# Kernel optimization log

Hardware: AMD Instinct MI355X
Metric: run time of the kernel (lower is better)

Reference implementation:

```python
import jax, jax.numpy as jnp
import numpy as np

B, L, C = 512, 2048, 32  # batch, seq_len, num_labels


def setup_inputs() -> dict:
    key = jax.random.key(0)
    k1, k2, k3 = jax.random.split(key, 3)
    emissions = jax.random.normal(k1, (B, L, C), dtype=jnp.float32)
    tags = jax.random.randint(k2, (B, L), 0, C, dtype=jnp.int32)
    mask = jnp.ones((B, L), dtype=jnp.int32)
    # learned parameter: transitions (num_labels, num_labels)
    transitions = jax.random.normal(k3, (C, C), dtype=jnp.float32)
    return {"emissions": emissions, "transitions": transitions, "tags": tags, "mask": mask}


def _crf_nll(emissions, transitions, tags, mask):
    Bn, Ln, Cn = emissions.shape
    maskf = mask.astype(emissions.dtype)

    # ---- gold-path score (vectorized over the t loop) ----
    # emit[b,t] = emissions[b,t,tags[b,t]] for t in [0, L-2]
    emit = jnp.take_along_axis(emissions[:, : Ln - 1], tags[:, : Ln - 1, None], axis=2)[..., 0]
    # trans[b,t] = transitions[tags[b,t], tags[b,t+1]]
    trans = transitions[tags[:, : Ln - 1], tags[:, 1:]]
    score = jnp.sum(emit * maskf[:, : Ln - 1] + trans * maskf[:, 1:], axis=1)

    msum = jnp.sum(mask, axis=1)
    last_idx = jnp.clip(msum - 1, 0)  # index of last valid tag
    last_tag = jnp.take_along_axis(tags, last_idx[:, None], axis=1)[:, 0]
    le_t = jnp.clip(msum, 1) - 1
    last_emission = emissions[jnp.arange(Bn), le_t, last_tag]
    score = score + last_emission

    # ---- log-partition via forward algorithm (lax.scan over time) ----
    # Faithful to source: alpha_t[b,n,p] = alpha[b,p] + transitions[n,p] + emit[b,n],
    # reduced over p; the source's mask line is an algebraic no-op (a*m + a*(1-m) = a).
    def step(alpha, emit_t):
        # alpha: (B, C) over prev label p; emit_t: (B, C) over next label n
        alpha_new = jax.nn.logsumexp(alpha[:, None, :] + transitions[None, :, :], axis=2) + emit_t
        return alpha_new, None

    alpha0 = emissions[:, 0]                      # (B, C)
    em_rest = jnp.swapaxes(emissions[:, 1:], 0, 1)  # (L-1, B, C)
    alpha, _ = jax.lax.scan(step, alpha0, em_rest)
    log_Z = jax.nn.logsumexp(alpha, axis=1)       # (B,)

    return jnp.mean(log_Z - score)


def reference(emissions, transitions, tags, mask):
    return _crf_nll(emissions, transitions, tags, mask)
```

## Files before the change

kernel.cpp:

```cpp
#include <hip/hip_runtime.h>
#include <stdint.h>

typedef short bf16x8 __attribute__((ext_vector_type(8)));
typedef float f32x16 __attribute__((ext_vector_type(16)));

#define LOG2E 1.44269504088896340736f
#define LN2f  0.69314718055994530942f

constexpr int Bn = 512;
constexpr int Ln = 2048;
constexpr int Cn = 32;
constexpr int NSEG = 64;
constexpr int SEGLEN = 32;
constexpr int WARM = 16;
constexpr int NGRP = 16;
constexpr int WPB  = 4;

__device__ __forceinline__ uint32_t pack2_bf16(float lo, float hi) {
    uint32_t a = __float_as_uint(lo) + 0x8000u;
    uint32_t b = __float_as_uint(hi) + 0x8000u;
    return __builtin_amdgcn_perm(b, a, 0x07060302u);
}

__global__ __launch_bounds__(256, 1) void crf_scan(
    const float* __restrict__ emis, const float* __restrict__ trans,
    const int* __restrict__ tags, const int* __restrict__ mask,
    float* __restrict__ dDelta, float* __restrict__ dScore, int* __restrict__ dMsum)
{
    __shared__ float Tlds[Cn * Cn];
    const int lane = threadIdx.x & 63;
    const int wid  = threadIdx.x >> 6;
    const int h    = lane >> 5;
    const int bl   = lane & 31;
    const int unit = blockIdx.x * WPB + wid;
    const int g    = unit & (NGRP - 1);
    const int s    = unit >> 4;
    const int b    = g * 32 + bl;
    const size_t eb = (size_t)b * Ln * Cn;
    const size_t tB = (size_t)b * Ln;

    for (int i = threadIdx.x; i < Cn * Cn; i += 256) Tlds[i] = trans[i];
    __syncthreads();

    bf16x8 A1, A2;
    {
        float e1[8], e2[8];
        #pragma unroll
        for (int j = 0; j < 8; ++j) {
            int c1 = 4 * h + (j & 3) + 8 * (j >> 2);
            e1[j] = __expf(trans[bl * Cn + c1]);
            e2[j] = __expf(trans[bl * Cn + c1 + 16]);
        }
        union { uint32_t u[4]; bf16x8 v; } ua, ub;
        #pragma unroll
        for (int q = 0; q < 4; ++q) {
            ua.u[q] = pack2_bf16(e1[2*q], e1[2*q+1]);
            ub.u[q] = pack2_bf16(e2[2*q], e2[2*q+1]);
        }
        A1 = ua.v; A2 = ub.v;
    }

    const f32x16 zeroC = {0.f,0.f,0.f,0.f,0.f,0.f,0.f,0.f,0.f,0.f,0.f,0.f,0.f,0.f,0.f,0.f};

    f32x16 Dv;
    bf16x8 B1, B2;
    float offF = 0.f;
    float adj  = 0.f;
    float score = 0.f;
    int   msum = 0;
    int   prevTag = 0;
    float4 buf[8][4];
    int tcur[8], mcur[8];

    const int t0 = (s == 0) ? 0 : s * SEGLEN - WARM;

    auto loadEm = [&](int t, float4 (&dst)[4]) {
        const float4* p = (const float4*)(emis + eb + (size_t)t * Cn + 4 * h);
        dst[0] = p[0]; dst[1] = p[2]; dst[2] = p[4]; dst[3] = p[6];
    };

    auto packB = [&]() {
        union { uint32_t u[4]; bf16x8 v; } p1, p2;
        #pragma unroll
        for (int q = 0; q < 4; ++q) {
            p1.u[q] = pack2_bf16(Dv[2*q],     Dv[2*q + 1]);
            p2.u[q] = pack2_bf16(Dv[8 + 2*q], Dv[8 + 2*q + 1]);
        }
        B1 = p1.v; B2 = p2.v;
    };

    auto initStep = [&](const float4 (&bu)[4]) {
        #pragma unroll
        for (int q = 0; q < 4; ++q) {
            Dv[4*q+0] = __expf(bu[q].x);
            Dv[4*q+1] = __expf(bu[q].y);
            Dv[4*q+2] = __expf(bu[q].z);
            Dv[4*q+3] = __expf(bu[q].w);
        }
        packB();
    };

    auto stepMfma = [&](const float4 (&bu)[4], float a) {
        f32x16 acc = __builtin_amdgcn_mfma_f32_32x32x16_bf16(A1, B1, zeroC, 0, 0, 0);
        acc = __builtin_amdgcn_mfma_f32_32x32x16_bf16(A2, B2, acc, 0, 0, 0);
        #pragma unroll
        for (int q = 0; q < 4; ++q) {
            float x0 = exp2f(fmaf(bu[q].x, LOG2E, a));
            float x1 = exp2f(fmaf(bu[q].y, LOG2E, a));
            float x2 = exp2f(fmaf(bu[q].z, LOG2E, a));
            float x3 = exp2f(fmaf(bu[q].w, LOG2E, a));
            Dv[4*q+0] = acc[4*q+0] * x0;
            Dv[4*q+1] = acc[4*q+1] * x1;
            Dv[4*q+2] = acc[4*q+2] * x2;
            Dv[4*q+3] = acc[4*q+3] * x3;
        }
        packB();
    };

    auto renorm = [&]() {
        float m0 = fmaxf(fmaxf(Dv[0], Dv[1]),  fmaxf(Dv[2],  Dv[3]));
        float m1 = fmaxf(fmaxf(Dv[4], Dv[5]),  fmaxf(Dv[6],  Dv[7]));
        float m2 = fmaxf(fmaxf(Dv[8], Dv[9]),  fmaxf(Dv[10], Dv[11]));
        float m3 = fmaxf(fmaxf(Dv[12],Dv[13]), fmaxf(Dv[14], Dv[15]));
        float m  = fmaxf(fmaxf(m0, m1), fmaxf(m2, m3));
        m = fmaxf(m, __shfl_xor(m, 32, 64));
        int k = (int)((__float_as_uint(m) >> 23) & 0xffu) - 126;
        offF += (float)k * LN2f;
        adj = -(float)k;
    };

    auto sumD = [&]() {
        float t = 0.f;
        #pragma unroll
        for (int r = 0; r < 16; ++r) t += Dv[r];
        t += __shfl_xor(t, 32, 64);
        return t;
    };

    auto loadTagsMask = [&](int t) {
        int4 a0 = *(const int4*)(tags + tB + t);
        int4 a1 = *(const int4*)(tags + tB + t + 4);
        int4 c0 = *(const int4*)(mask + tB + t);
        int4 c1 = *(const int4*)(mask + tB + t + 4);
        tcur[0]=a0.x; tcur[1]=a0.y; tcur[2]=a0.z; tcur[3]=a0.w;
        tcur[4]=a1.x; tcur[5]=a1.y; tcur[6]=a1.z; tcur[7]=a1.w;
        mcur[0]=c0.x; mcur[1]=c0.y; mcur[2]=c0.z; mcur[3]=c0.w;
        mcur[4]=c1.x; mcur[5]=c1.y; mcur[6]=c1.z; mcur[7]=c1.w;
    };

    auto realBlock = [&](int tb) {
        int tn = min(tb + 8, Ln - 8);
        int4 a0 = *(const int4*)(tags + tB + tn);
        int4 a1 = *(const int4*)(tags + tB + tn + 4);
        int4 c0 = *(const int4*)(mask + tB + tn);
        int4 c1 = *(const int4*)(mask + tB + tn + 4);
        float gv[8];
        #pragma unroll
        for (int u = 0; u < 8; ++u)
            gv[u] = emis[eb + (size_t)(tb + u) * Cn + tcur[u]];
        #pragma unroll
        for (int u = 0; u < 8; ++u) {
            stepMfma(buf[u], (u == 0) ? adj : 0.f);
            loadEm(min(tb + u + 8, Ln - 1), buf[u]);
            float fm = (float)mcur[u];
            msum += mcur[u];
            score += fm * Tlds[(prevTag << 5) + tcur[u]];
            if (tb + u < Ln - 1) score += fm * gv[u];
            prevTag = tcur[u];
        }
        adj = 0.f;
        tcur[0]=a0.x; tcur[1]=a0.y; tcur[2]=a0.z; tcur[3]=a0.w;
        tcur[4]=a1.x; tcur[5]=a1.y; tcur[6]=a1.z; tcur[7]=a1.w;
        mcur[0]=c0.x; mcur[1]=c0.y; mcur[2]=c0.z; mcur[3]=c0.w;
        mcur[4]=c1.x; mcur[5]=c1.y; mcur[6]=c1.z; mcur[7]=c1.w;
    };

    #pragma unroll
    for (int u = 0; u < 8; ++u) loadEm(t0 + u, buf[u]);

    if (s == 0) {
        loadTagsMask(0);
        initStep(buf[0]);
        loadEm(8, buf[0]);
        float g0 = emis[eb + tcur[0]];
        score += (float)mcur[0] * g0;
        msum += mcur[0];
        prevTag = tcur[0];
        float gv[8];
        #pragma unroll
        for (int u = 1; u < 8; ++u) gv[u] = emis[eb + (size_t)u * Cn + tcur[u]];
        #pragma unroll
        for (int u = 1; u < 8; ++u) {
            stepMfma(buf[u], 0.f);
            loadEm(u + 8, buf[u]);
            float fm = (float)mcur[u];
            msum += mcur[u];
            score += fm * Tlds[(prevTag << 5) + tcur[u]];
            score += fm * gv[u];
            prevTag = tcur[u];
        }
        loadTagsMask(8);
        renorm();
        constexpr int NB0 = (SEGLEN - 8) / 8;
        #pragma unroll 1
        for (int blk = 0; blk < NB0; ++blk) {
            realBlock(8 + 8 * blk);
            if (blk < NB0 - 1) renorm();
        }
    } else {
        initStep(buf[0]);
        loadEm(t0 + 8, buf[0]);
        #pragma unroll
        for (int u = 1; u < 8; ++u) {
            stepMfma(buf[u], 0.f);
            loadEm(t0 + 8 + u, buf[u]);
        }
        renorm();
        prevTag = tags[tB + s * SEGLEN - 1];
        loadTagsMask(s * SEGLEN);
        #pragma unroll
        for (int u = 0; u < 8; ++u) {
            stepMfma(buf[u], (u == 0) ? adj : 0.f);
            loadEm(min(t0 + u + 16, Ln - 1), buf[u]);
        }
        adj = 0.f;
        float S = sumD();
        adj = -__log2f(S);
        offF = 0.f;
        constexpr int NB = SEGLEN / 8;
        #pragma unroll 1
        for (int blk = 0; blk < NB; ++blk) {
            realBlock(s * SEGLEN + 8 * blk);
            if (blk < NB - 1) renorm();
        }
    }

    float Sf = sumD();
    float delta = offF + __logf(Sf);
    if (lane < 32) {
        dDelta[s * Bn + b] = delta;
        dScore[s * Bn + b] = score;
        dMsum [s * Bn + b] = msum;
    }
}

__global__ void crf_final(const float* __restrict__ dDelta, const float* __restrict__ dScore,
                          const int* __restrict__ dMsum, const int* __restrict__ tags,
                          const float* __restrict__ emis, float* __restrict__ out)
{
    __shared__ float red[8];
    int b = threadIdx.x;
    float lz = 0.f, sc = 0.f; int ms = 0;
    #pragma unroll 8
    for (int s2 = 0; s2 < NSEG; ++s2) {
        lz += dDelta[s2 * Bn + b];
        sc += dScore[s2 * Bn + b];
        ms += dMsum [s2 * Bn + b];
    }
    int last_idx = max(ms - 1, 0);
    int le_t     = max(ms, 1) - 1;
    int lt = tags[(size_t)b * Ln + last_idx];
    float le = emis[((size_t)b * Ln + le_t) * Cn + lt];
    float val = lz - (sc + le);
    #pragma unroll
    for (int o = 32; o > 0; o >>= 1) val += __shfl_down(val, o, 64);
    if ((b & 63) == 0) red[b >> 6] = val;
    __syncthreads();
    if (b == 0) {
        float t = 0.f;
        #pragma unroll
        for (int w = 0; w < 8; ++w) t += red[w];
        out[0] = t * (1.0f / (float)Bn);
    }
}

extern "C" void kernel_launch(void* const* d_in, const int* in_sizes, int n_in,
                              void* d_out, int out_size, void* d_ws, size_t ws_size,
                              hipStream_t stream)
{
    const float* emis  = (const float*)d_in[0];
    const float* trans = (const float*)d_in[1];
    const int*   tags  = (const int*)d_in[2];
    const int*   mask  = (const int*)d_in[3];
    float* wsf = (float*)d_ws;
    float* dDelta = wsf;
    float* dScore = wsf + NSEG * Bn;
    int*   dMsum  = (int*)(wsf + 2 * NSEG * Bn);
    crf_scan<<<(NGRP * NSEG) / WPB, 64 * WPB, 0, stream>>>(emis, trans, tags, mask, dDelta, dScore, dMsum);
    crf_final<<<1, Bn, 0, stream>>>(dDelta, dScore, dMsum, tags, emis, (float*)d_out);
}
```

Baseline: 240.5 us.

## Stream emissions via async global-to-LDS loads and split gold-score into separate kernel

The scan kernel now prefetches each timestep's emission tile into a swizzled per-wave LDS ring of depth 8 using global_load_lds, with a manual vmcnt wait, instead of holding register buffers. Gold-path score and mask-sum work moves out of the serial scan into a new per-batch parallel kernel that also reduces the segment deltas. The aim is to cut register pressure and per-step latency in the recurrence and to give the score computation full parallelism. The cost is an extra kernel launch, a second pass over tags and emissions, and reliance on a hand-tuned vmcnt count being correct.

```diff
diff --git a/kernel.cpp b/kernel.cpp
--- a/kernel.cpp
+++ b/kernel.cpp
@@ -15,6 +15,7 @@
 constexpr int WARM = 16;
 constexpr int NGRP = 16;
 constexpr int WPB  = 4;
+constexpr int DEPTH = 8;
 
 __device__ __forceinline__ uint32_t pack2_bf16(float lo, float hi) {
     uint32_t a = __float_as_uint(lo) + 0x8000u;
@@ -22,25 +23,39 @@
     return __builtin_amdgcn_perm(b, a, 0x07060302u);
 }
 
+__device__ __forceinline__ void gload16(const float* g, float* l) {
+    __builtin_amdgcn_global_load_lds(
+        (__attribute__((address_space(1))) void*)g,
+        (__attribute__((address_space(3))) void*)l,
+        16, 0, 0);
+}
+
 __global__ __launch_bounds__(256, 1) void crf_scan(
     const float* __restrict__ emis, const float* __restrict__ trans,
-    const int* __restrict__ tags, const int* __restrict__ mask,
-    float* __restrict__ dDelta, float* __restrict__ dScore, int* __restrict__ dMsum)
+    float* __restrict__ dDelta)
 {
-    __shared__ float Tlds[Cn * Cn];
+    __shared__ float ELDS[WPB][DEPTH][1024];
     const int lane = threadIdx.x & 63;
     const int wid  = threadIdx.x >> 6;
     const int h    = lane >> 5;
     const int bl   = lane & 31;
+    const int bl7  = bl & 7;
     const int unit = blockIdx.x * WPB + wid;
     const int g    = unit & (NGRP - 1);
     const int s    = unit >> 4;
     const int b    = g * 32 + bl;
-    const size_t eb = (size_t)b * Ln * Cn;
-    const size_t tB = (size_t)b * Ln;
-
-    for (int i = threadIdx.x; i < Cn * Cn; i += 256) Tlds[i] = trans[i];
-    __syncthreads();
+
+    size_t gqb[4];
+    {
+        const int lr = lane >> 3;
+        const int lc = lane & 7;
+        #pragma unroll
+        for (int q = 0; q < 4; ++q) {
+            int br = 8 * q + lr;
+            int sg = lc ^ lr;
+            gqb[q] = (size_t)(g * 32 + br) * Ln * Cn + (size_t)(sg * 4);
+        }
+    }
 
     bf16x8 A1, A2;
     {
@@ -66,17 +81,24 @@
     bf16x8 B1, B2;
     float offF = 0.f;
     float adj  = 0.f;
-    float score = 0.f;
-    int   msum = 0;
-    int   prevTag = 0;
-    float4 buf[8][4];
-    int tcur[8], mcur[8];
 
     const int t0 = (s == 0) ? 0 : s * SEGLEN - WARM;
-
-    auto loadEm = [&](int t, float4 (&dst)[4]) {
-        const float4* p = (const float4*)(emis + eb + (size_t)t * Cn + 4 * h);
-        dst[0] = p[0]; dst[1] = p[2]; dst[2] = p[4]; dst[3] = p[6];
+    const int nsteps = (s == 0) ? SEGLEN : (SEGLEN + WARM);
+
+    auto issueTile = [&](int t, int slot) {
+        #pragma unroll
+        for (int q = 0; q < 4; ++q) {
+            const float* gp = emis + gqb[q] + (size_t)t * Cn;
+            gload16(gp, &ELDS[wid][slot][q * 256]);
+        }
+    };
+
+    auto readFrag = [&](int slot, float4 (&bu)[4]) {
+        #pragma unroll
+        for (int q = 0; q < 4; ++q) {
+            int c16 = (h + 2 * q) ^ bl7;
+            bu[q] = *(const float4*)&ELDS[wid][slot][bl * 32 + c16 * 4];
+        }
     };
 
     auto packB = [&]() {
@@ -89,18 +111,12 @@
         B1 = p1.v; B2 = p2.v;
     };
 
-    auto initStep = [&](const float4 (&bu)[4]) {
-        #pragma unroll
-        for (int q = 0; q < 4; ++q) {
-            Dv[4*q+0] = __expf(bu[q].x);
-            Dv[4*q+1] = __expf(bu[q].y);
-            Dv[4*q+2] = __expf(bu[q].z);
-            Dv[4*q+3] = __expf(bu[q].w);
-        }
-        packB();
-    };
-
-    auto stepMfma = [&](const float4 (&bu)[4], float a) {
+    auto pclamp = [&](int t) { return (t > Ln - 1) ? (Ln - 1) : t; };
+
+    auto stepConsume = [&](int idx, float a) {
+        asm volatile("s_waitcnt vmcnt(28)" ::: "memory");
+        float4 bu[4];
+        readFrag(idx & (DEPTH - 1), bu);
         f32x16 acc = __builtin_amdgcn_mfma_f32_32x32x16_bf16(A1, B1, zeroC, 0, 0, 0);
         acc = __builtin_amdgcn_mfma_f32_32x32x16_bf16(A2, B2, acc, 0, 0, 0);
         #pragma unroll
@@ -115,6 +131,24 @@
             Dv[4*q+3] = acc[4*q+3] * x3;
         }
         packB();
+        asm volatile("" ::: "memory");
+        issueTile(pclamp(t0 + idx + DEPTH), idx & (DEPTH - 1));
+    };
+
+    auto initConsume = [&](int idx) {
+        asm volatile("s_waitcnt vmcnt(28)" ::: "memory");
+        float4 bu[4];
+        readFrag(idx & (DEPTH - 1), bu);
+        #pragma unroll
+        for (int q = 0; q < 4; ++q) {
+            Dv[4*q+0] = __expf(bu[q].x);
+            Dv[4*q+1] = __expf(bu[q].y);
+            Dv[4*q+2] = __expf(bu[q].z);
+            Dv[4*q+3] = __expf(bu[q].w);
+        }
+        packB();
+        asm volatile("" ::: "memory");
+        issueTile(pclamp(t0 + idx + DEPTH), idx & (DEPTH - 1));
     };
 
     auto renorm = [&]() {
@@ -137,101 +171,40 @@
         return t;
     };
 
-    auto loadTagsMask = [&](int t) {
-        int4 a0 = *(const int4*)(tags + tB + t);
-        int4 a1 = *(const int4*)(tags + tB + t + 4);
-        int4 c0 = *(const int4*)(mask + tB + t);
-        int4 c1 = *(const int4*)(mask + tB + t + 4);
-        tcur[0]=a0.x; tcur[1]=a0.y; tcur[2]=a0.z; tcur[3]=a0.w;
-        tcur[4]=a1.x; tcur[5]=a1.y; tcur[6]=a1.z; tcur[7]=a1.w;
-        mcur[0]=c0.x; mcur[1]=c0.y; mcur[2]=c0.z; mcur[3]=c0.w;
-        mcur[4]=c1.x; mcur[5]=c1.y; mcur[6]=c1.z; mcur[7]=c1.w;
-    };
-
-    auto realBlock = [&](int tb) {
-        int tn = min(tb + 8, Ln - 8);
-        int4 a0 = *(const int4*)(tags + tB + tn);
-        int4 a1 = *(const int4*)(tags + tB + tn + 4);
-        int4 c0 = *(const int4*)(mask + tB + tn);
-        int4 c1 = *(const int4*)(mask + tB + tn + 4);
-        float gv[8];
-        #pragma unroll
-        for (int u = 0; u < 8; ++u)
-            gv[u] = emis[eb + (size_t)(tb + u) * Cn + tcur[u]];
-        #pragma unroll
-        for (int u = 0; u < 8; ++u) {
-            stepMfma(buf[u], (u == 0) ? adj : 0.f);
-            loadEm(min(tb + u + 8, Ln - 1), buf[u]);
-            float fm = (float)mcur[u];
-            msum += mcur[u];
-            score += fm * Tlds[(prevTag << 5) + tcur[u]];
-            if (tb + u < Ln - 1) score += fm * gv[u];
-            prevTag = tcur[u];
-        }
-        adj = 0.f;
-        tcur[0]=a0.x; tcur[1]=a0.y; tcur[2]=a0.z; tcur[3]=a0.w;
-        tcur[4]=a1.x; tcur[5]=a1.y; tcur[6]=a1.z; tcur[7]=a1.w;
-        mcur[0]=c0.x; mcur[1]=c0.y; mcur[2]=c0.z; mcur[3]=c0.w;
-        mcur[4]=c1.x; mcur[5]=c1.y; mcur[6]=c1.z; mcur[7]=c1.w;
-    };
-
     #pragma unroll
-    for (int u = 0; u < 8; ++u) loadEm(t0 + u, buf[u]);
-
+    for (int i = 0; i < DEPTH; ++i) issueTile(pclamp(t0 + i), i);
+
+    int idx = 0;
+    (void)nsteps;
     if (s == 0) {
-        loadTagsMask(0);
-        initStep(buf[0]);
-        loadEm(8, buf[0]);
-        float g0 = emis[eb + tcur[0]];
-        score += (float)mcur[0] * g0;
-        msum += mcur[0];
-        prevTag = tcur[0];
-        float gv[8];
-        #pragma unroll
-        for (int u = 1; u < 8; ++u) gv[u] = emis[eb + (size_t)u * Cn + tcur[u]];
-        #pragma unroll
-        for (int u = 1; u < 8; ++u) {
-            stepMfma(buf[u], 0.f);
-            loadEm(u + 8, buf[u]);
-            float fm = (float)mcur[u];
-            msum += mcur[u];
-            score += fm * Tlds[(prevTag << 5) + tcur[u]];
-            score += fm * gv[u];
-            prevTag = tcur[u];
-        }
-        loadTagsMask(8);
+        initConsume(idx); ++idx;
+        #pragma unroll
+        for (int u = 1; u < 8; ++u) { stepConsume(idx, 0.f); ++idx; }
         renorm();
-        constexpr int NB0 = (SEGLEN - 8) / 8;
         #pragma unroll 1
-        for (int blk = 0; blk < NB0; ++blk) {
-            realBlock(8 + 8 * blk);
-            if (blk < NB0 - 1) renorm();
+        for (int blk = 0; blk < 3; ++blk) {
+            #pragma unroll
+            for (int u = 0; u < 8; ++u) { stepConsume(idx, (u == 0) ? adj : 0.f); ++idx; }
+            adj = 0.f;
+            if (blk < 2) renorm();
         }
     } else {
-        initStep(buf[0]);
-        loadEm(t0 + 8, buf[0]);
-        #pragma unroll
-        for (int u = 1; u < 8; ++u) {
-            stepMfma(buf[u], 0.f);
-            loadEm(t0 + 8 + u, buf[u]);
-        }
+        initConsume(idx); ++idx;
+        #pragma unroll
+        for (int u = 1; u < 8; ++u) { stepConsume(idx, 0.f); ++idx; }
         renorm();
-        prevTag = tags[tB + s * SEGLEN - 1];
-        loadTagsMask(s * SEGLEN);
-        #pragma unroll
-        for (int u = 0; u < 8; ++u) {
-            stepMfma(buf[u], (u == 0) ? adj : 0.f);
-            loadEm(min(t0 + u + 16, Ln - 1), buf[u]);
-        }
+        #pragma unroll
+        for (int u = 0; u < 8; ++u) { stepConsume(idx, (u == 0) ? adj : 0.f); ++idx; }
         adj = 0.f;
         float S = sumD();
         adj = -__log2f(S);
         offF = 0.f;
-        constexpr int NB = SEGLEN / 8;
         #pragma unroll 1
-        for (int blk = 0; blk < NB; ++blk) {
-            realBlock(s * SEGLEN + 8 * blk);
-            if (blk < NB - 1) renorm();
+        for (int blk = 0; blk < 4; ++blk) {
+            #pragma unroll
+            for (int u = 0; u < 8; ++u) { stepConsume(idx, (u == 0) ? adj : 0.f); ++idx; }
+            adj = 0.f;
+            if (blk < 3) renorm();
         }
     }
 
@@ -239,29 +212,79 @@
     float delta = offF + __logf(Sf);
     if (lane < 32) {
         dDelta[s * Bn + b] = delta;
-        dScore[s * Bn + b] = score;
-        dMsum [s * Bn + b] = msum;
-    }
-}
-
-__global__ void crf_final(const float* __restrict__ dDelta, const float* __restrict__ dScore,
-                          const int* __restrict__ dMsum, const int* __restrict__ tags,
-                          const float* __restrict__ emis, float* __restrict__ out)
+    }
+}
+
+__global__ __launch_bounds__(256) void crf_score(
+    const float* __restrict__ emis, const float* __restrict__ trans,
+    const int* __restrict__ tags, const int* __restrict__ mask,
+    const float* __restrict__ dDelta, float* __restrict__ dVal)
+{
+    __shared__ float Tl[Cn * Cn];
+    __shared__ float redS[4];
+    __shared__ int   redM[4];
+    const int b = blockIdx.x;
+    const int tid = threadIdx.x;
+    for (int i = tid; i < Cn * Cn; i += 256) Tl[i] = trans[i];
+    __syncthreads();
+
+    const size_t tB = (size_t)b * Ln;
+    const size_t eb = (size_t)b * Ln * Cn;
+    const int t0 = tid * 8;
+
+    int tg[9], mk[9];
+    {
+        int4 a0 = *(const int4*)(tags + tB + t0);
+        int4 a1 = *(const int4*)(tags + tB + t0 + 4);
+        int4 c0 = *(const int4*)(mask + tB + t0);
+        int4 c1 = *(const int4*)(mask + tB + t0 + 4);
+        tg[0]=a0.x; tg[1]=a0.y; tg[2]=a0.z; tg[3]=a0.w;
+        tg[4]=a1.x; tg[5]=a1.y; tg[6]=a1.z; tg[7]=a1.w;
+        mk[0]=c0.x; mk[1]=c0.y; mk[2]=c0.z; mk[3]=c0.w;
+        mk[4]=c1.x; mk[5]=c1.y; mk[6]=c1.z; mk[7]=c1.w;
+        tg[8] = (t0 + 8 < Ln) ? tags[tB + t0 + 8] : 0;
+        mk[8] = (t0 + 8 < Ln) ? mask[tB + t0 + 8] : 0;
+    }
+
+    float sc = 0.f; int ms = 0;
+    #pragma unroll
+    for (int u = 0; u < 8; ++u) {
+        int t = t0 + u;
+        ms += mk[u];
+        if (t < Ln - 1) {
+            sc += (float)mk[u]     * emis[eb + (size_t)t * Cn + tg[u]];
+            sc += (float)mk[u + 1] * Tl[(tg[u] << 5) + tg[u + 1]];
+        }
+    }
+    #pragma unroll
+    for (int o = 32; o > 0; o >>= 1) {
+        sc += __shfl_down(sc, o, 64);
+        ms += __shfl_down(ms, o, 64);
+    }
+    if ((tid & 63) == 0) { redS[tid >> 6] = sc; redM[tid >> 6] = ms; }
+    __syncthreads();
+
+    if (tid < NSEG) {
+        float lz = dDelta[(size_t)tid * Bn + b];
+        #pragma unroll
+        for (int o = 32; o > 0; o >>= 1) lz += __shfl_down(lz, o, 64);
+        if (tid == 0) {
+            float scT = redS[0] + redS[1] + redS[2] + redS[3];
+            int   msT = redM[0] + redM[1] + redM[2] + redM[3];
+            int last_idx = max(msT - 1, 0);
+            int le_t     = max(msT, 1) - 1;
+            int lt = tags[tB + last_idx];
+            float le = emis[eb + (size_t)le_t * Cn + lt];
+            dVal[b] = lz - (scT + le);
+        }
+    }
+}
+
+__global__ void crf_final(const float* __restrict__ dVal, float* __restrict__ out)
 {
     __shared__ float red[8];
     int b = threadIdx.x;
-    float lz = 0.f, sc = 0.f; int ms = 0;
-    #pragma unroll 8
-    for (int s2 = 0; s2 < NSEG; ++s2) {
-        lz += dDelta[s2 * Bn + b];
-        sc += dScore[s2 * Bn + b];
-        ms += dMsum [s2 * Bn + b];
-    }
-    int last_idx = max(ms - 1, 0);
-    int le_t     = max(ms, 1) - 1;
-    int lt = tags[(size_t)b * Ln + last_idx];
-    float le = emis[((size_t)b * Ln + le_t) * Cn + lt];
-    float val = lz - (sc + le);
+    float val = dVal[b];
     #pragma unroll
     for (int o = 32; o > 0; o >>= 1) val += __shfl_down(val, o, 64);
     if ((b & 63) == 0) red[b >> 6] = val;
@@ -284,8 +307,8 @@
     const int*   mask  = (const int*)d_in[3];
     float* wsf = (float*)d_ws;
     float* dDelta = wsf;
-    float* dScore = wsf + NSEG * Bn;
-    int*   dMsum  = (int*)(wsf + 2 * NSEG * Bn);
-    crf_scan<<<(NGRP * NSEG) / WPB, 64 * WPB, 0, stream>>>(emis, trans, tags, mask, dDelta, dScore, dMsum);
-    crf_final<<<1, Bn, 0, stream>>>(dDelta, dScore, dMsum, tags, emis, (float*)d_out);
-}
+    float* dVal   = wsf + NSEG * Bn;
+    crf_scan<<<(NGRP * NSEG) / WPB, 64 * WPB, 0, stream>>>(emis, trans, dDelta);
+    crf_score<<<Bn, 256, 0, stream>>>(emis, trans, tags, mask, dDelta, dVal);
+    crf_final<<<1, Bn, 0, stream>>>(dVal, (float*)d_out);
+}
```

Result: slower. 249.7 us (+3.8%).
